# Optimization experiments

Hardware: AMD Instinct MI355X
Metric: run time of the kernel (lower is better)

## Reference

```python
import jax, jax.numpy as jnp
import numpy as np

N = 100_000      # nodes
E = 1_250_000    # edges (avg degree ~12.5)
D_IN, D_H, D_OUT = 64, 64, 64


def setup_inputs() -> dict:
    key = jax.random.key(0)
    ks = jax.random.split(key, 7)
    x = jax.random.normal(ks[0], (N, D_IN), dtype=jnp.float32)
    edge_index = jax.random.randint(ks[1], (2, E), 0, N, dtype=jnp.int32)
    edge_weight = jax.random.uniform(ks[2], (E,), dtype=jnp.float32)
    # GCNConv linear weights: PyG lin stores [out, in], applied as x @ W.T; bias added after aggregation.
    W1 = jax.random.normal(ks[3], (D_H, D_IN), dtype=jnp.float32) * (1.0 / np.sqrt(D_IN))
    b1 = jax.random.normal(ks[4], (D_H,), dtype=jnp.float32) * 0.01
    W2 = jax.random.normal(ks[5], (D_OUT, D_H), dtype=jnp.float32) * (1.0 / np.sqrt(D_H))
    b2 = jax.random.normal(ks[6], (D_OUT,), dtype=jnp.float32) * 0.01
    return {"x": x, "edge_index": edge_index, "edge_weight": edge_weight,
            "W1": W1, "b1": b1, "W2": W2, "b2": b2}


def _gcn_conv(x, src, dst, w, W, b, n_nodes):
    # PyG GCNConv: add self-loops (weight 1), symmetric normalization, linear, scatter-add, +bias.
    deg = jax.ops.segment_sum(w, dst, num_segments=n_nodes) + 1.0  # +1 from self-loop
    dis = jnp.where(deg > 0, jax.lax.rsqrt(deg), 0.0)              # deg^{-1/2}
    coef = dis[src] * w * dis[dst]                                 # per-edge norm, [E]
    h = x @ W.T                                                    # [N, out]
    agg = jax.ops.segment_sum(h[src] * coef[:, None], dst, num_segments=n_nodes)
    agg = agg + h * (dis * dis)[:, None]                           # self-loop: dis_i * 1 * dis_i
    return agg + b


def reference(x, edge_index, edge_weight, W1, b1, W2, b2):
    n = x.shape[0]
    src, dst = edge_index[0], edge_index[1]
    h = _gcn_conv(x, src, dst, edge_weight, W1, b1, n)
    h = jax.nn.relu(h)
    # dropout p=0.0 -> identity
    return _gcn_conv(h, src, dst, edge_weight, W2, b2, n)
```

## Files before the change

kernel.cpp:

```cpp
#include <hip/hip_runtime.h>


typedef unsigned int u32;
typedef unsigned short u16;

#define NBKT 256
#define LSH 9
#define BNODES 512
#define SRCBITS 17
#define SRCMASK ((1u << SRCBITS) - 1u)

__device__ inline u16 f2bf(float f) {
  u32 u = __float_as_uint(f);
  u32 r = u + 0x7FFFu + ((u >> 16) & 1u);
  return (u16)(r >> 16);
}
__device__ inline float bf_lo(u32 p) { return __uint_as_float(p << 16); }
__device__ inline float bf_hi(u32 p) { return __uint_as_float(p & 0xFFFF0000u); }

__device__ inline u32 blockscan256_excl(u32 val, u32* wsum) {
  int lane = threadIdx.x & 63, wv = threadIdx.x >> 6;
  u32 inc = val;
  #pragma unroll
  for (int d = 1; d < 64; d <<= 1) {
    u32 t = __shfl_up(inc, d);
    if (lane >= d) inc += t;
  }
  if (lane == 63) wsum[wv] = inc;
  __syncthreads();
  u32 off = 0;
  #pragma unroll
  for (int i = 0; i < 4; ++i) if (i < wv) off += wsum[i];
  return off + inc - val;
}

__global__ void k_bin(const int* __restrict__ ei, u32* __restrict__ blockcnt,
                      int E, int chunk) {
  __shared__ u32 hist[NBKT];
  if (threadIdx.x < NBKT) hist[threadIdx.x] = 0u;
  __syncthreads();
  int e0 = blockIdx.x * chunk;
  int e1 = min(E, e0 + chunk);
  for (int e = e0 + (threadIdx.x << 1); e < e1; e += 512) {
    if (e + 1 < e1) {
      int2 dd = *(const int2*)(ei + E + e);
      atomicAdd(&hist[dd.x >> LSH], 1u);
      atomicAdd(&hist[dd.y >> LSH], 1u);
    } else {
      atomicAdd(&hist[ei[E + e] >> LSH], 1u);
    }
  }
  __syncthreads();
  if (threadIdx.x < NBKT)
    blockcnt[threadIdx.x * 256 + blockIdx.x] = hist[threadIdx.x];
}

__global__ void k_scan_rows(u32* __restrict__ blockcnt, u32* __restrict__ bucket_total) {
  int wid = blockIdx.x * 4 + (threadIdx.x >> 6);
  int lane = threadIdx.x & 63;
  u32* row = blockcnt + (size_t)wid * 256;
  uint4 v = ((uint4*)row)[lane];
  u32 s = v.x + v.y + v.z + v.w;
  u32 inc = s;
  #pragma unroll
  for (int d = 1; d < 64; d <<= 1) {
    u32 t = __shfl_up(inc, d);
    if (lane >= d) inc += t;
  }
  u32 excl = inc - s;
  uint4 o;
  o.x = excl; o.y = excl + v.x; o.z = o.y + v.y; o.w = o.z + v.z;
  ((uint4*)row)[lane] = o;
  if (lane == 63) bucket_total[wid] = inc;
}

__global__ void k_scan_buckets(const u32* __restrict__ bucket_total,
                               u32* __restrict__ bucket_start) {
  __shared__ u32 wsum[4];
  int t = threadIdx.x;
  u32 v = bucket_total[t];
  u32 excl = blockscan256_excl(v, wsum);
  bucket_start[t] = excl;
  if (t == 255) bucket_start[256] = excl + v;
}

__global__ __launch_bounds__(256, 4) void k_scatter_gemm(
    const int* __restrict__ ei, const float* __restrict__ w,
    const u32* __restrict__ blockcnt, const u32* __restrict__ bucket_start,
    uint2* __restrict__ bucketed,
    const float* __restrict__ X, const float* __restrict__ W,
    u16* __restrict__ H, int N, int E, int chunk) {
  __shared__ float Wt[64 * 65];
  __shared__ float Xs[16 * 64];
  __shared__ u32 base[NBKT];
  int tid = threadIdx.x;
  if ((int)blockIdx.x < 256) {
    if (tid < NBKT)
      base[tid] = blockcnt[(size_t)tid * 256 + blockIdx.x] + bucket_start[tid];
    __syncthreads();
    int e0 = blockIdx.x * chunk, e1 = min(E, e0 + chunk);
    for (int e = e0 + (tid << 1); e < e1; e += 512) {
      if (e + 1 < e1) {
        int2 ss = *(const int2*)(ei + e);
        int2 dd = *(const int2*)(ei + E + e);
        float2 wv = *(const float2*)(w + e);
        u32 p0 = atomicAdd(&base[dd.x >> LSH], 1u);
        u32 p1 = atomicAdd(&base[dd.y >> LSH], 1u);
        bucketed[p0] = make_uint2((u32)ss.x | ((u32)(dd.x & (BNODES - 1)) << SRCBITS),
                                  __float_as_uint(wv.x));
        bucketed[p1] = make_uint2((u32)ss.y | ((u32)(dd.y & (BNODES - 1)) << SRCBITS),
                                  __float_as_uint(wv.y));
      } else {
        int s = ei[e], d = ei[E + e];
        u32 pos = atomicAdd(&base[d >> LSH], 1u);
        bucketed[pos] = make_uint2((u32)s | ((u32)(d & (BNODES - 1)) << SRCBITS),
                                   __float_as_uint(w[e]));
      }
    }
    return;
  }
  int row0 = ((int)blockIdx.x - 256) * 16;
  if (row0 >= N) return;
  for (int i = tid; i < 4096; i += 256) Wt[(i & 63) * 65 + (i >> 6)] = W[i];
  {
    const float4* xsrc = (const float4*)(X + (size_t)row0 * 64);
    if (row0 + 16 <= N) {
      ((float4*)Xs)[tid] = xsrc[tid];
    } else {
      int r = tid >> 4;
      ((float4*)Xs)[tid] = (row0 + r < N) ? xsrc[tid]
                                          : make_float4(0.f, 0.f, 0.f, 0.f);
    }
  }
  __syncthreads();
  int lane = tid & 63, wv4 = tid >> 6;
  int rbase = wv4 * 4;
  float a0 = 0.f, a1 = 0.f, a2 = 0.f, a3 = 0.f;
  #pragma unroll 4
  for (int k4 = 0; k4 < 16; ++k4) {
    int k = k4 << 2;
    float w0 = Wt[k * 65 + lane], w1 = Wt[(k + 1) * 65 + lane];
    float w2 = Wt[(k + 2) * 65 + lane], w3 = Wt[(k + 3) * 65 + lane];
    float4 xa = *(const float4*)&Xs[(rbase + 0) * 64 + k];
    float4 xb = *(const float4*)&Xs[(rbase + 1) * 64 + k];
    float4 xc = *(const float4*)&Xs[(rbase + 2) * 64 + k];
    float4 xd = *(const float4*)&Xs[(rbase + 3) * 64 + k];
    a0 = fmaf(xa.x, w0, fmaf(xa.y, w1, fmaf(xa.z, w2, fmaf(xa.w, w3, a0))));
    a1 = fmaf(xb.x, w0, fmaf(xb.y, w1, fmaf(xb.z, w2, fmaf(xb.w, w3, a1))));
    a2 = fmaf(xc.x, w0, fmaf(xc.y, w1, fmaf(xc.z, w2, fmaf(xc.w, w3, a2))));
    a3 = fmaf(xd.x, w0, fmaf(xd.y, w1, fmaf(xd.z, w2, fmaf(xd.w, w3, a3))));
  }
  int row = row0 + rbase;
  if (row + 3 < N) {
    H[(size_t)row * 64 + lane]       = f2bf(a0);
    H[(size_t)(row + 1) * 64 + lane] = f2bf(a1);
    H[(size_t)(row + 2) * 64 + lane] = f2bf(a2);
    H[(size_t)(row + 3) * 64 + lane] = f2bf(a3);
  } else {
    if (row < N)     H[(size_t)row * 64 + lane]       = f2bf(a0);
    if (row + 1 < N) H[(size_t)(row + 1) * 64 + lane] = f2bf(a1);
    if (row + 2 < N) H[(size_t)(row + 2) * 64 + lane] = f2bf(a2);
    if (row + 3 < N) H[(size_t)(row + 3) * 64 + lane] = f2bf(a3);
  }
}

__global__ void k_statsfill(const uint2* __restrict__ bucketed,
                            const u32* __restrict__ bucket_start,
                            float* __restrict__ dis, int4* __restrict__ info,
                            int2* __restrict__ csr, u16* __restrict__ H, int N) {
  __shared__ u32 hist[BNODES];
  __shared__ u32 cur[BNODES];
  __shared__ float disl[BNODES];
  __shared__ u32 wsum[4];
  int b = blockIdx.x, tid = threadIdx.x;
  for (int i = tid; i < BNODES; i += 256) hist[i] = 0u;
  __syncthreads();
  u32 s0 = bucket_start[b], s1 = bucket_start[b + 1];
  for (u32 p = s0 + tid; p < s1; p += 256) {
    uint2 ed = bucketed[p];
    u32 local = ed.x >> SRCBITS;
    u32 wfix = (u32)(__uint_as_float(ed.y) * 262144.0f);
    atomicAdd(&hist[local], (1u << 24) | wfix);
  }
  __syncthreads();
  u32 h0 = hist[2 * tid], h1 = hist[2 * tid + 1];
  u32 c0 = h0 >> 24, c1 = h1 >> 24;
  u32 excl = blockscan256_excl(c0 + c1, wsum);
  float d0 = rsqrtf(1.0f + (float)(h0 & 0xFFFFFFu) * (1.0f / 262144.0f));
  float d1 = rsqrtf(1.0f + (float)(h1 & 0xFFFFFFu) * (1.0f / 262144.0f));
  cur[2 * tid] = excl;
  cur[2 * tid + 1] = excl + c0;
  disl[2 * tid] = d0;
  disl[2 * tid + 1] = d1;
  int n0 = b * BNODES + 2 * tid;
  if (n0 < N) {
    dis[n0] = d0;
    info[n0] = make_int4((int)(s0 + excl), (int)c0, __float_as_int(d0), 0);
  }
  if (n0 + 1 < N) {
    dis[n0 + 1] = d1;
    info[n0 + 1] = make_int4((int)(s0 + excl + c0), (int)c1, __float_as_int(d1), 0);
  }
  __syncthreads();
  for (u32 p = s0 + tid; p < s1; p += 256) {
    uint2 ed = bucketed[p];
    u32 local = ed.x >> SRCBITS;
    u32 pos = atomicAdd(&cur[local], 1u);
    csr[s0 + pos] = make_int2((int)(ed.x & SRCMASK), (int)ed.y);
  }
  uint2* Hv = (uint2*)H;
  for (int i = tid; i < BNODES * 16; i += 256) {
    int row = i >> 4;
    int node = b * BNODES + row;
    if (node >= N) break;
    float dv = disl[row];
    size_t idx = (size_t)node * 16 + (i & 15);
    uint2 v = Hv[idx];
    u32 lo = (u32)f2bf(bf_lo(v.x) * dv) | ((u32)f2bf(bf_hi(v.x) * dv) << 16);
    u32 hi = (u32)f2bf(bf_lo(v.y) * dv) | ((u32)f2bf(bf_hi(v.y) * dv) << 16);
    Hv[idx] = make_uint2(lo, hi);
  }
}

__global__ __launch_bounds__(256, 4) void k_gemm(
    const float* __restrict__ X, const float* __restrict__ W,
    const float* __restrict__ dis, u16* __restrict__ H, int N) {
  __shared__ float Wt[64 * 65];
  __shared__ float Xs[16 * 64];
  int tid = threadIdx.x;
  int row0 = blockIdx.x * 16;
  if (row0 >= N) return;
  for (int i = tid; i < 4096; i += 256) Wt[(i & 63) * 65 + (i >> 6)] = W[i];
  {
    const float4* xsrc = (const float4*)(X + (size_t)row0 * 64);
    if (row0 + 16 <= N) {
      ((float4*)Xs)[tid] = xsrc[tid];
    } else {
      int r = tid >> 4;
      ((float4*)Xs)[tid] = (row0 + r < N) ? xsrc[tid]
                                          : make_float4(0.f, 0.f, 0.f, 0.f);
    }
  }
  __syncthreads();
  int lane = tid & 63, wv = tid >> 6;
  int rbase = wv * 4;
  float a0 = 0.f, a1 = 0.f, a2 = 0.f, a3 = 0.f;
  #pragma unroll 4
  for (int k4 = 0; k4 < 16; ++k4) {
    int k = k4 << 2;
    float w0 = Wt[k * 65 + lane], w1 = Wt[(k + 1) * 65 + lane];
    float w2 = Wt[(k + 2) * 65 + lane], w3 = Wt[(k + 3) * 65 + lane];
    float4 xa = *(const float4*)&Xs[(rbase + 0) * 64 + k];
    float4 xb = *(const float4*)&Xs[(rbase + 1) * 64 + k];
    float4 xc = *(const float4*)&Xs[(rbase + 2) * 64 + k];
    float4 xd = *(const float4*)&Xs[(rbase + 3) * 64 + k];
    a0 = fmaf(xa.x, w0, fmaf(xa.y, w1, fmaf(xa.z, w2, fmaf(xa.w, w3, a0))));
    a1 = fmaf(xb.x, w0, fmaf(xb.y, w1, fmaf(xb.z, w2, fmaf(xb.w, w3, a1))));
    a2 = fmaf(xc.x, w0, fmaf(xc.y, w1, fmaf(xc.z, w2, fmaf(xc.w, w3, a2))));
    a3 = fmaf(xd.x, w0, fmaf(xd.y, w1, fmaf(xd.z, w2, fmaf(xd.w, w3, a3))));
  }
  int row = row0 + rbase;
  if (row + 3 < N) {
    float dv0 = dis[row], dv1 = dis[row + 1], dv2 = dis[row + 2], dv3 = dis[row + 3];
    H[(size_t)row * 64 + lane]       = f2bf(a0 * dv0);
    H[(size_t)(row + 1) * 64 + lane] = f2bf(a1 * dv1);
    H[(size_t)(row + 2) * 64 + lane] = f2bf(a2 * dv2);
    H[(size_t)(row + 3) * 64 + lane] = f2bf(a3 * dv3);
  } else {
    if (row < N)     H[(size_t)row * 64 + lane]       = f2bf(a0 * dis[row]);
    if (row + 1 < N) H[(size_t)(row + 1) * 64 + lane] = f2bf(a1 * dis[row + 1]);
    if (row + 2 < N) H[(size_t)(row + 2) * 64 + lane] = f2bf(a2 * dis[row + 2]);
    if (row + 3 < N) H[(size_t)(row + 3) * 64 + lane] = f2bf(a3 * dis[row + 3]);
  }
}

template <int RELU>
__global__ __launch_bounds__(256, 6) void k_aggregate(
    const u16* __restrict__ H, const int4* __restrict__ info,
    const int2* __restrict__ csr, const float* __restrict__ bias,
    float* __restrict__ Y, int N) {
  int node = blockIdx.x * 4 + (threadIdx.x >> 6);
  if (node >= N) return;
  int lane = threadIdx.x & 63;
  int eg = lane >> 4;
  int fid = (lane & 15) << 2;
  int4 nfo = info[node];
  int s0 = nfo.x, n = nfo.y;
  float d = __int_as_float(nfo.z);
  uint2 hs = *(const uint2*)(H + (size_t)node * 64 + fid);
  float4 b4 = *(const float4*)(bias + fid);
  float4 acc = make_float4(0.f, 0.f, 0.f, 0.f);
  int nm1 = n - 1;
  for (int base = 0; base < n; base += 16) {
    int p0 = base + eg;
    int q0 = min(p0, nm1), q1 = min(p0 + 4, nm1);
    int q2 = min(p0 + 8, nm1), q3 = min(p0 + 12, nm1);
    int2 c0 = csr[s0 + q0];
    int2 c1 = csr[s0 + q1];
    int2 c2 = csr[s0 + q2];
    int2 c3 = csr[s0 + q3];
    uint2 h0 = *(const uint2*)(H + (size_t)c0.x * 64 + fid);
    uint2 h1 = *(const uint2*)(H + (size_t)c1.x * 64 + fid);
    uint2 h2 = *(const uint2*)(H + (size_t)c2.x * 64 + fid);
    uint2 h3 = *(const uint2*)(H + (size_t)c3.x * 64 + fid);
    float f0 = (p0      < n) ? __int_as_float(c0.y) : 0.f;
    float f1 = (p0 + 4  < n) ? __int_as_float(c1.y) : 0.f;
    float f2 = (p0 + 8  < n) ? __int_as_float(c2.y) : 0.f;
    float f3 = (p0 + 12 < n) ? __int_as_float(c3.y) : 0.f;
    acc.x = fmaf(bf_lo(h0.x), f0, acc.x); acc.y = fmaf(bf_hi(h0.x), f0, acc.y);
    acc.z = fmaf(bf_lo(h0.y), f0, acc.z); acc.w = fmaf(bf_hi(h0.y), f0, acc.w);
    acc.x = fmaf(bf_lo(h1.x), f1, acc.x); acc.y = fmaf(bf_hi(h1.x), f1, acc.y);
    acc.z = fmaf(bf_lo(h1.y), f1, acc.z); acc.w = fmaf(bf_hi(h1.y), f1, acc.w);
    acc.x = fmaf(bf_lo(h2.x), f2, acc.x); acc.y = fmaf(bf_hi(h2.x), f2, acc.y);
    acc.z = fmaf(bf_lo(h2.y), f2, acc.z); acc.w = fmaf(bf_hi(h2.y), f2, acc.w);
    acc.x = fmaf(bf_lo(h3.x), f3, acc.x); acc.y = fmaf(bf_hi(h3.x), f3, acc.y);
    acc.z = fmaf(bf_lo(h3.y), f3, acc.z); acc.w = fmaf(bf_hi(h3.y), f3, acc.w);
  }
  acc.x += __shfl_xor(acc.x, 16); acc.y += __shfl_xor(acc.y, 16);
  acc.z += __shfl_xor(acc.z, 16); acc.w += __shfl_xor(acc.w, 16);
  acc.x += __shfl_xor(acc.x, 32); acc.y += __shfl_xor(acc.y, 32);
  acc.z += __shfl_xor(acc.z, 32); acc.w += __shfl_xor(acc.w, 32);
  if (eg == 0) {
    acc.x = (acc.x + bf_lo(hs.x)) * d + b4.x;
    acc.y = (acc.y + bf_hi(hs.x)) * d + b4.y;
    acc.z = (acc.z + bf_lo(hs.y)) * d + b4.z;
    acc.w = (acc.w + bf_hi(hs.y)) * d + b4.w;
    if (RELU) {
      acc.x = fmaxf(acc.x, 0.f); acc.y = fmaxf(acc.y, 0.f);
      acc.z = fmaxf(acc.z, 0.f); acc.w = fmaxf(acc.w, 0.f);
    }
    *(float4*)(Y + (size_t)node * 64 + fid) = acc;
  }
}

extern "C" void kernel_launch(void* const* d_in, const int* in_sizes, int n_in,
                              void* d_out, int out_size, void* d_ws, size_t ws_size,
                              hipStream_t stream) {
  const float* x  = (const float*)d_in[0];
  const int*   ei = (const int*)d_in[1];
  const float* w  = (const float*)d_in[2];
  const float* W1 = (const float*)d_in[3];
  const float* b1 = (const float*)d_in[4];
  const float* W2 = (const float*)d_in[5];
  const float* b2 = (const float*)d_in[6];
  const int N = in_sizes[0] / 64;
  const int E = in_sizes[2];

  char* ws = (char*)d_ws;
  size_t off = 0;
  auto alloc = [&](size_t bytes) -> char* {
    char* p = ws + off;
    off = (off + bytes + 255) & ~(size_t)255;
    return p;
  };
  u32*   blockcnt     = (u32*)  alloc((size_t)NBKT * 256 * 4);
  u32*   bucket_total = (u32*)  alloc((size_t)NBKT * 4);
  u32*   bucket_start = (u32*)  alloc((size_t)(NBKT + 1) * 4);
  uint2* bucketed     = (uint2*)alloc((size_t)E * 8);
  int2*  csr          = (int2*) alloc((size_t)E * 8);
  float* dis          = (float*)alloc((size_t)N * 4);
  int4*  info         = (int4*) alloc((size_t)N * 16);
  u16*   h1           = (u16*)  alloc((size_t)N * 64 * 2);
  u16*   h2           = (u16*)  alloc((size_t)N * 64 * 2);
  float* ybuf         = (float*)d_out;

  const int chunk = ((E + 511) / 512) * 2;
  const int nbG = (N + 15) / 16;
  const int nbB = (N + BNODES - 1) >> LSH;

  k_bin<<<256, 256, 0, stream>>>(ei, blockcnt, E, chunk);
  k_scan_rows<<<NBKT / 4, 256, 0, stream>>>(blockcnt, bucket_total);
  k_scan_buckets<<<1, 256, 0, stream>>>(bucket_total, bucket_start);
  k_scatter_gemm<<<256 + nbG, 256, 0, stream>>>(ei, w, blockcnt, bucket_start,
                                                bucketed, x, W1, h1, N, E, chunk);
  k_statsfill<<<nbB, 256, 0, stream>>>(bucketed, bucket_start, dis, info, csr, h1, N);

  k_aggregate<1><<<(N + 3) / 4, 256, 0, stream>>>(h1, info, csr, b1, ybuf, N);
  k_gemm<<<nbG, 256, 0, stream>>>(ybuf, W2, dis, h2, N);
  k_aggregate<0><<<(N + 3) / 4, 256, 0, stream>>>(h2, info, csr, b2, (float*)d_out, N);
}
```

Measured before the change: 257.6 us.

## Map 16 lanes per node in aggregation, loop edges serially, drop shuffle reduction

The aggregation kernel now assigns a 16-lane group to each node (16 nodes per block) instead of a full wavefront split into four edge groups. Each group walks its edge list four edges at a time, which removes the cross-lane shuffle reduction and the lanes left idle on low-degree nodes. Launch bounds are raised to allow more resident blocks. The trade-off is fewer independent gathers in flight per node and divergence when nodes in the same wave have different degrees.

```diff
diff --git a/kernel.cpp b/kernel.cpp
--- a/kernel.cpp
+++ b/kernel.cpp
@@ -275,27 +275,26 @@
 }
 
 template <int RELU>
-__global__ __launch_bounds__(256, 6) void k_aggregate(
+__global__ __launch_bounds__(256, 8) void k_aggregate(
     const u16* __restrict__ H, const int4* __restrict__ info,
     const int2* __restrict__ csr, const float* __restrict__ bias,
     float* __restrict__ Y, int N) {
-  int node = blockIdx.x * 4 + (threadIdx.x >> 6);
-  if (node >= N) return;
-  int lane = threadIdx.x & 63;
-  int eg = lane >> 4;
-  int fid = (lane & 15) << 2;
-  int4 nfo = info[node];
+  int tid = threadIdx.x;
+  int node = blockIdx.x * 16 + (tid >> 4);
+  int fid = (tid & 15) << 2;
+  bool valid = node < N;
+  int4 nfo = valid ? info[node] : make_int4(0, 0, 0, 0);
   int s0 = nfo.x, n = nfo.y;
   float d = __int_as_float(nfo.z);
-  uint2 hs = *(const uint2*)(H + (size_t)node * 64 + fid);
+  uint2 hs = valid ? *(const uint2*)(H + (size_t)node * 64 + fid)
+                   : make_uint2(0u, 0u);
   float4 b4 = *(const float4*)(bias + fid);
   float4 acc = make_float4(0.f, 0.f, 0.f, 0.f);
   int nm1 = n - 1;
-  for (int base = 0; base < n; base += 16) {
-    int p0 = base + eg;
-    int q0 = min(p0, nm1), q1 = min(p0 + 4, nm1);
-    int q2 = min(p0 + 8, nm1), q3 = min(p0 + 12, nm1);
-    int2 c0 = csr[s0 + q0];
+  for (int base = 0; base < n; base += 4) {
+    int q1 = min(base + 1, nm1);
+    int q2 = min(base + 2, nm1), q3 = min(base + 3, nm1);
+    int2 c0 = csr[s0 + base];
     int2 c1 = csr[s0 + q1];
     int2 c2 = csr[s0 + q2];
     int2 c3 = csr[s0 + q3];
@@ -303,10 +302,10 @@
     uint2 h1 = *(const uint2*)(H + (size_t)c1.x * 64 + fid);
     uint2 h2 = *(const uint2*)(H + (size_t)c2.x * 64 + fid);
     uint2 h3 = *(const uint2*)(H + (size_t)c3.x * 64 + fid);
-    float f0 = (p0      < n) ? __int_as_float(c0.y) : 0.f;
-    float f1 = (p0 + 4  < n) ? __int_as_float(c1.y) : 0.f;
-    float f2 = (p0 + 8  < n) ? __int_as_float(c2.y) : 0.f;
-    float f3 = (p0 + 12 < n) ? __int_as_float(c3.y) : 0.f;
+    float f0 = __int_as_float(c0.y);
+    float f1 = (base + 1 < n) ? __int_as_float(c1.y) : 0.f;
+    float f2 = (base + 2 < n) ? __int_as_float(c2.y) : 0.f;
+    float f3 = (base + 3 < n) ? __int_as_float(c3.y) : 0.f;
     acc.x = fmaf(bf_lo(h0.x), f0, acc.x); acc.y = fmaf(bf_hi(h0.x), f0, acc.y);
     acc.z = fmaf(bf_lo(h0.y), f0, acc.z); acc.w = fmaf(bf_hi(h0.y), f0, acc.w);
     acc.x = fmaf(bf_lo(h1.x), f1, acc.x); acc.y = fmaf(bf_hi(h1.x), f1, acc.y);
@@ -316,11 +315,7 @@
     acc.x = fmaf(bf_lo(h3.x), f3, acc.x); acc.y = fmaf(bf_hi(h3.x), f3, acc.y);
     acc.z = fmaf(bf_lo(h3.y), f3, acc.z); acc.w = fmaf(bf_hi(h3.y), f3, acc.w);
   }
-  acc.x += __shfl_xor(acc.x, 16); acc.y += __shfl_xor(acc.y, 16);
-  acc.z += __shfl_xor(acc.z, 16); acc.w += __shfl_xor(acc.w, 16);
-  acc.x += __shfl_xor(acc.x, 32); acc.y += __shfl_xor(acc.y, 32);
-  acc.z += __shfl_xor(acc.z, 32); acc.w += __shfl_xor(acc.w, 32);
-  if (eg == 0) {
+  if (valid) {
     acc.x = (acc.x + bf_lo(hs.x)) * d + b4.x;
     acc.y = (acc.y + bf_hi(hs.x)) * d + b4.y;
     acc.z = (acc.z + bf_lo(hs.y)) * d + b4.z;
@@ -366,6 +361,7 @@
 
   const int chunk = ((E + 511) / 512) * 2;
   const int nbG = (N + 15) / 16;
+  const int nbA = (N + 15) / 16;
   const int nbB = (N + BNODES - 1) >> LSH;
 
   k_bin<<<256, 256, 0, stream>>>(ei, blockcnt, E, chunk);
@@ -375,7 +371,7 @@
                                                 bucketed, x, W1, h1, N, E, chunk);
   k_statsfill<<<nbB, 256, 0, stream>>>(bucketed, bucket_start, dis, info, csr, h1, N);
 
-  k_aggregate<1><<<(N + 3) / 4, 256, 0, stream>>>(h1, info, csr, b1, ybuf, N);
+  k_aggregate<1><<<nbA, 256, 0, stream>>>(h1, info, csr, b1, ybuf, N);
   k_gemm<<<nbG, 256, 0, stream>>>(ybuf, W2, dis, h2, N);
-  k_aggregate<0><<<(N + 3) / 4, 256, 0, stream>>>(h2, info, csr, b2, (float*)d_out, N);
-}
+  k_aggregate<0><<<nbA, 256, 0, stream>>>(h2, info, csr, b2, (float*)d_out, N);
+}
```

Result: faster. 245.2 us (-4.8%).
